# Kernel tuning notes

Hardware: AMD Instinct MI355X
Metric: run time of the kernel (lower is better)

Reference implementation:

```python
import jax, jax.numpy as jnp
import numpy as np

IMG_H = IMG_W = 640
NUM_CLASSES = 80
B = 8
NUM_ANCHORS = 76725
MAX_TOTAL = 200          # max_total_size == max_size_per_class
SCORE_TH = 0.5
IOU_TH = 0.5
K_CAND = 256             # per-class candidate pool for NMS (>= max survivors)
VARIANCES = jnp.asarray([0.1, 0.1, 0.2, 0.2], jnp.float32)


def _build_anchors(img_h, img_w):
    # RetinaNet AnchorBox: levels 3..7, 3 ratios x 3 scales, [cx, cy, w, h]
    ratios = [0.5, 1.0, 2.0]
    scales = [2.0 ** x for x in (0.0, 1.0 / 3.0, 2.0 / 3.0)]
    areas = [s * s for s in (32.0, 64.0, 128.0, 256.0, 512.0)]
    out = []
    for lvl, stride in enumerate([2 ** i for i in range(3, 8)]):
        dims = []
        for r in ratios:
            h = np.sqrt(areas[lvl] / r)
            w = areas[lvl] / h
            for s in scales:
                dims.append([w * s, h * s])
        dims = np.asarray(dims, np.float32)                      # [9,2]
        fh = int(np.ceil(img_h / stride)); fw = int(np.ceil(img_w / stride))
        rx = (np.arange(fw, dtype=np.float32) + 0.5) * stride
        ry = (np.arange(fh, dtype=np.float32) + 0.5) * stride
        cx, cy = np.meshgrid(rx, ry)
        centers = np.broadcast_to(np.stack([cx, cy], -1)[:, :, None, :], (fh, fw, 9, 2))
        d = np.broadcast_to(dims[None, None], (fh, fw, 9, 2))
        out.append(np.concatenate([centers, d], -1).reshape(-1, 4))
    return jnp.asarray(np.concatenate(out, 0))                   # [A,4]


def setup_inputs() -> dict:
    key = jax.random.key(0)
    k1, k2 = jax.random.split(key)
    box_pred = jax.random.normal(k1, (B, NUM_ANCHORS, 4), jnp.float32)
    cls_pred = jax.random.normal(k2, (B, NUM_ANCHORS, NUM_CLASSES), jnp.float32)
    anchor_boxes = _build_anchors(IMG_H, IMG_W)
    return {"box_pred": box_pred, "cls_pred": cls_pred, "anchor_boxes": anchor_boxes}


def _iou_one_vs_many(box, boxes):
    # box [4] vs boxes [K,4] in corner format
    lt = jnp.maximum(box[:2], boxes[:, :2])
    rb = jnp.minimum(box[2:], boxes[:, 2:])
    wh = jnp.maximum(rb - lt, 0.0)
    inter = wh[:, 0] * wh[:, 1]
    a1 = (box[2] - box[0]) * (box[3] - box[1])
    a2 = (boxes[:, 2] - boxes[:, 0]) * (boxes[:, 3] - boxes[:, 1])
    return inter / jnp.maximum(a1 + a2 - inter, 1e-8)


def _nms_keep(boxes, scores):
    # boxes [K,4] already sorted by descending score; greedy NMS
    eligible = scores > SCORE_TH
    idx = jnp.arange(K_CAND)

    def body(i, keep):
        iou = _iou_one_vs_many(boxes[i], boxes)
        suppress = (iou > IOU_TH) & (idx > i)
        return jnp.where(keep[i], keep & ~suppress, keep)

    keep = jax.lax.fori_loop(0, K_CAND, body, eligible)
    keep = keep & ((jnp.cumsum(keep) - 1) < MAX_TOTAL)           # max_size_per_class cap
    return keep


def _decode_and_nms(box_pred, cls_pred, anchor_boxes):
    scores_all = jax.nn.sigmoid(cls_pred)                        # [B,A,C]
    # decode: (dx,dy,dw,dh)*variances against [cx,cy,w,h] anchors
    d = box_pred * VARIANCES
    xy = d[..., :2] * anchor_boxes[None, :, 2:] + anchor_boxes[None, :, :2]
    wh = jnp.exp(d[..., 2:]) * anchor_boxes[None, :, 2:]
    boxes = jnp.concatenate([xy - 0.5 * wh, xy + 0.5 * wh], -1)  # [B,A,4] corners

    sc = jnp.swapaxes(scores_all, 1, 2)                          # [B,C,A]
    top_sc, top_idx = jax.lax.top_k(sc, K_CAND)                  # [B,C,K] sorted desc
    cand_boxes = jnp.take_along_axis(boxes[:, None], top_idx[..., None], axis=2)  # [B,C,K,4]

    keep = jax.lax.stop_gradient(jax.vmap(jax.vmap(_nms_keep))(cand_boxes, top_sc))  # [B,C,K]
    sel = jnp.where(keep, top_sc, -1.0)

    flat_sc = sel.reshape(B, -1)                                 # [B,C*K]
    flat_boxes = cand_boxes.reshape(B, -1, 4)
    flat_lbl = jnp.broadcast_to(jnp.arange(NUM_CLASSES)[None, :, None],
                                (B, NUM_CLASSES, K_CAND)).reshape(B, -1)

    fs, fi = jax.lax.top_k(flat_sc, MAX_TOTAL)                   # combine across classes
    out_boxes = jnp.take_along_axis(flat_boxes, fi[..., None], axis=1)
    out_lbl = jnp.take_along_axis(flat_lbl, fi, axis=1).astype(jnp.float32)
    valid = fs > 0.0                                             # pad invalid slots
    return (jnp.where(valid[..., None], out_boxes, 0.0),
            jnp.where(valid, fs, 0.0),
            jnp.where(valid, out_lbl, -1.0))


def reference(box_pred, cls_pred, anchor_boxes):
    return _decode_and_nms(box_pred, cls_pred, anchor_boxes)
```

## Files before the change

kernel.cpp:

```cpp
#include <hip/hip_runtime.h>
#include <math.h>
#include <stdint.h>

typedef unsigned long long u64;
typedef unsigned int u32;

#define NB 8
#define NA 76725
#define NC 80
#define KC 256
#define MAXT 200
#define CAP 2048
#define SELCAP 768
#define TAU 2.0f
#define CHUNK 512
#define NCHUNK 150
#define BCAP 48
#define CSTRIDE 16

#define OFF_BUFA      0ull
#define OFF_CLASSLIST 10485760ull
#define OFF_CANDBOX   11796480ull
#define OFF_COUNTS    14417920ull

__device__ __forceinline__ void kf_proc(float4 v, int i, int a0,
                                        u64 (*bucket)[BCAP], u32* bcnt) {
  int a = a0 + i / (NC / 4);
  int c0 = (i % (NC / 4)) * 4;
  float vv[4] = {v.x, v.y, v.z, v.w};
#pragma unroll
  for (int j = 0; j < 4; j++) {
    if (vv[j] > TAU) {
      int c = c0 + j;
      u32 pos = atomicAdd(&bcnt[c], 1u);
      if (pos < BCAP)
        bucket[c][pos] = ((u64)__float_as_uint(vv[j]) << 32) | (u32)a;
    }
  }
}

__global__ __launch_bounds__(256) void kfilter(const float* __restrict__ cls,
                                               u64* __restrict__ bufA,
                                               u32* __restrict__ counts) {
  __shared__ u64 bucket[NC][BCAP];
  __shared__ u32 bcnt[NC];
  __shared__ u32 gbase[NC];
  __shared__ u32 pref[NC + 1];

  const int b = blockIdx.x / NCHUNK;
  const int ch = blockIdx.x % NCHUNK;
  const int tid = threadIdx.x;
  const int a0 = ch * CHUNK;
  const int aN = (NA - a0) < CHUNK ? (NA - a0) : CHUNK;

  for (int i = tid; i < NC; i += 256) bcnt[i] = 0;
  __syncthreads();

  const float4* p = (const float4*)(cls + ((size_t)b * NA + a0) * NC);
  const int n4 = aN * (NC / 4);
  for (int i0 = tid; i0 < n4; i0 += 2048) {
    float4 v[8];
    bool g[8];
#pragma unroll
    for (int u = 0; u < 8; u++) {
      g[u] = (i0 + u * 256) < n4;
      if (g[u]) v[u] = p[i0 + u * 256];
    }
#pragma unroll
    for (int u = 0; u < 8; u++)
      if (g[u]) kf_proc(v[u], i0 + u * 256, a0, bucket, bcnt);
  }
  __syncthreads();
  if (tid < NC) {
    u32 n = bcnt[tid];
    if (n > BCAP) n = BCAP;
    bcnt[tid] = n;
    gbase[tid] = atomicAdd(&counts[(b * NC + tid) * CSTRIDE], n);
  }
  __syncthreads();
  if (tid == 0) {
    u32 s = 0;
    for (int c = 0; c < NC; c++) { pref[c] = s; s += bcnt[c]; }
    pref[NC] = s;
  }
  __syncthreads();
  const int total = (int)pref[NC];
  for (int e = tid; e < total; e += 256) {
    int lo = 0, hi = NC;
    while (lo + 1 < hi) { int mid = (lo + hi) >> 1; if ((int)pref[mid] <= e) lo = mid; else hi = mid; }
    int c = lo;
    int loc = e - (int)pref[c];
    u32 gb = gbase[c] + (u32)loc;
    if (gb < CAP)
      bufA[((size_t)(b * NC + c)) * CAP + gb] = bucket[c][loc];
  }
}

__global__ __launch_bounds__(256) void kselect(
    const float* __restrict__ cls, const float* __restrict__ boxp,
    const float* __restrict__ anc, u64* __restrict__ bufA,
    const u32* __restrict__ counts, u64* __restrict__ classList,
    float4* __restrict__ candBox) {
  __shared__ u64 sbuf[CAP];
  __shared__ u32 hist[1024];
  __shared__ u64 sel[SELCAP];
  __shared__ u64 skey[KC];
  __shared__ u64 scolT[4][KC];
  __shared__ float4 sBox[KC];
  __shared__ float sAr[KC];
  __shared__ int sNsel, sExtra, sSb;

  const int tid = threadIdx.x;
  const int bc = blockIdx.x;
  const int b = bc / NC, c = bc % NC;
  u64* buf = bufA + (size_t)bc * CAP;

  int cnt0 = (int)counts[bc * CSTRIDE];
  if (cnt0 > CAP) cnt0 = CAP;
  int cnt = cnt0;
  if (cnt0 < KC) {
    if (tid == 0) sExtra = 0;
    __syncthreads();
    for (int a = tid; a < NA; a += 256) {
      float x = cls[((size_t)b * NA + a) * NC + c];
      if (x > 0.0f && !(x > TAU)) {
        int pos = cnt0 + atomicAdd(&sExtra, 1);
        if (pos < CAP) buf[pos] = ((u64)__float_as_uint(x) << 32) | (u32)a;
      }
    }
    __syncthreads();
    cnt = cnt0 + sExtra;
  }
  if (cnt > CAP) cnt = CAP;

  for (int i = tid; i < 1024; i += 256) hist[i] = 0;
  if (tid == 0) sNsel = 0;
  skey[tid] = 0;
  for (int e = tid; e < cnt; e += 256) sbuf[e] = buf[e];
  __syncthreads();

  for (int e = tid; e < cnt; e += 256) {
    float f = __uint_as_float((u32)(sbuf[e] >> 32));
    int bin = (int)(f * 170.0f);
    bin = bin < 0 ? 0 : (bin > 1023 ? 1023 : bin);
    atomicAdd(&hist[bin], 1u);
  }
  __syncthreads();

  if (tid < 64) {
    int s = 0;
#pragma unroll
    for (int i = 0; i < 16; i++) s += (int)hist[tid * 16 + i];
    int suf = s;
#pragma unroll
    for (int d = 1; d < 64; d <<= 1) {
      int t = __shfl_down(suf, d, 64);
      if (tid + d < 64) suf += t;
    }
    u64 mask = __ballot(suf >= KC);
    int sb = mask ? (63 - __clzll((long long)mask)) : 0;
    if (tid == 0) sSb = sb;
  }
  __syncthreads();
  const int sb = sSb;

  for (int e = tid; e < cnt; e += 256) {
    u64 k = sbuf[e];
    float f = __uint_as_float((u32)(k >> 32));
    int bin = (int)(f * 170.0f);
    bin = bin < 0 ? 0 : (bin > 1023 ? 1023 : bin);
    if ((bin >> 4) >= sb) {
      float sc = 1.0f / (1.0f + expf(-f));
      u32 a = (u32)k;
      int pos = atomicAdd(&sNsel, 1);
      if (pos < SELCAP)
        sel[pos] = ((u64)__float_as_uint(sc) << 32) | (0xFFFFFFFFu - a);
    }
  }
  __syncthreads();
  int nsel = sNsel;
  if (nsel > SELCAP) nsel = SELCAP;

  for (int e = tid; e < nsel; e += 256) {
    u64 k = sel[e];
    int r = 0;
    for (int q = 0; q < nsel; q++) r += (sel[q] > k) ? 1 : 0;
    if (r < KC) skey[r] = k;
  }
  __syncthreads();

  {
    u64 k = skey[tid];
    u32 a = 0xFFFFFFFFu - (u32)k;
    if (k == 0ull || a >= NA) a = 0;
    float4 p = ((const float4*)boxp)[(size_t)b * NA + a];
    float4 an = ((const float4*)anc)[a];
    float dx = __fmul_rn(p.x, 0.1f), dy = __fmul_rn(p.y, 0.1f);
    float dw = __fmul_rn(p.z, 0.2f), dh = __fmul_rn(p.w, 0.2f);
    float cx = __fadd_rn(__fmul_rn(dx, an.z), an.x);
    float cy = __fadd_rn(__fmul_rn(dy, an.w), an.y);
    float w = __fmul_rn(expf(dw), an.z);
    float h = __fmul_rn(expf(dh), an.w);
    float4 bx;
    bx.x = __fsub_rn(cx, __fmul_rn(0.5f, w));
    bx.y = __fsub_rn(cy, __fmul_rn(0.5f, h));
    bx.z = __fadd_rn(cx, __fmul_rn(0.5f, w));
    bx.w = __fadd_rn(cy, __fmul_rn(0.5f, h));
    sBox[tid] = bx;
    sAr[tid] = __fmul_rn(__fsub_rn(bx.z, bx.x), __fsub_rn(bx.w, bx.y));
    candBox[(size_t)bc * KC + tid] = bx;
  }
  __syncthreads();

  {
    const int j = tid;
    float4 bj = sBox[j];
    float aj = sAr[j];
    u64 cw[4] = {0ull, 0ull, 0ull, 0ull};
    for (int i = 0; i < j; i++) {
      float4 bi = sBox[i];
      float ai = sAr[i];
      float lx = fmaxf(bi.x, bj.x), ly = fmaxf(bi.y, bj.y);
      float rx = fminf(bi.z, bj.z), ry = fminf(bi.w, bj.w);
      float wx = fmaxf(__fsub_rn(rx, lx), 0.0f);
      float wy = fmaxf(__fsub_rn(ry, ly), 0.0f);
      float inter = __fmul_rn(wx, wy);
      float uni = fmaxf(__fsub_rn(__fadd_rn(ai, aj), inter), 1e-8f);
      float iou = __fdiv_rn(inter, uni);
      if (iou > 0.5f) cw[i >> 6] |= (1ull << (i & 63));
    }
#pragma unroll
    for (int w = 0; w < 4; w++) scolT[w][j] = cw[w];
  }
  __syncthreads();

  if (tid < 64) {
    const int ln = tid;
    u64 C[4][4];
#pragma unroll
    for (int s = 0; s < 4; s++)
#pragma unroll
      for (int w = 0; w < 4; w++) C[s][w] = scolT[w][s * 64 + ln];
    int keep = 0;
#pragma unroll
    for (int s = 0; s < 4; s++)
      if (skey[s * 64 + ln] != 0ull) keep |= (1 << s);
#pragma unroll
    for (int w = 0; w < 4; w++) {
      u64 c0 = C[0][w], c1 = C[1][w], c2 = C[2][w], c3 = C[3][w];
      for (int t = 0; t < 64; t++) {
        int kt = __shfl(keep, t, 64);
        if ((kt >> w) & 1) {
          int sup = (int)((c0 >> t) & 1) | ((int)((c1 >> t) & 1) << 1) |
                    ((int)((c2 >> t) & 1) << 2) | ((int)((c3 >> t) & 1) << 3);
          keep &= ~sup;
        }
      }
    }
    u64 m[4];
#pragma unroll
    for (int s = 0; s < 4; s++) m[s] = __ballot((keep >> s) & 1);
    int tot = 0;
#pragma unroll
    for (int s = 0; s < 4; s++) tot += __popcll(m[s]);
    int keptTotal = tot < MAXT ? tot : MAXT;
    u64 lmask = (1ull << ln) - 1ull;
    int base = 0;
#pragma unroll
    for (int s = 0; s < 4; s++) {
      int j = s * 64 + ln;
      int cum = base + (int)__popcll(m[s] & lmask);
      if (((keep >> s) & 1) && cum < MAXT) {
        u64 hi = skey[j] >> 32;
        classList[(size_t)bc * KC + cum] =
            (hi << 32) | (u64)(0xFFFFFFFFu - (u32)(c * KC + j));
      }
      base += (int)__popcll(m[s]);
    }
    for (int t2 = ln; t2 < KC; t2 += 64)
      if (t2 >= keptTotal) classList[(size_t)bc * KC + t2] = 0;
  }
}

__device__ __forceinline__ u64 shfl64(u64 v, int src) {
  int lo = __shfl((int)(u32)v, src, 64);
  int hi = __shfl((int)(v >> 32), src, 64);
  return ((u64)(u32)hi << 32) | (u32)lo;
}
__device__ __forceinline__ u64 shflxor64(u64 v, int mask) {
  int lo = __shfl_xor((int)(u32)v, mask, 64);
  int hi = __shfl_xor((int)(v >> 32), mask, 64);
  return ((u64)(u32)hi << 32) | (u32)lo;
}
#define CSWAP(a, b) { if ((a) < (b)) { u64 _t = (a); (a) = (b); (b) = _t; } }

__device__ __forceinline__ void wave_merge(u64 acc[4], const u64 cur[4], int ln) {
  u64 t0 = shfl64(cur[3], 63 - ln);
  u64 t1 = shfl64(cur[2], 63 - ln);
  u64 t2 = shfl64(cur[1], 63 - ln);
  u64 t3 = shfl64(cur[0], 63 - ln);
  acc[0] = acc[0] > t0 ? acc[0] : t0;
  acc[1] = acc[1] > t1 ? acc[1] : t1;
  acc[2] = acc[2] > t2 ? acc[2] : t2;
  acc[3] = acc[3] > t3 ? acc[3] : t3;
  CSWAP(acc[0], acc[2]); CSWAP(acc[1], acc[3]);
  CSWAP(acc[0], acc[1]); CSWAP(acc[2], acc[3]);
#pragma unroll
  for (int s = 32; s >= 1; s >>= 1) {
#pragma unroll
    for (int k = 0; k < 4; k++) {
      u64 o = shflxor64(acc[k], s);
      u64 mx = acc[k] > o ? acc[k] : o;
      u64 mn = acc[k] < o ? acc[k] : o;
      acc[k] = ((ln & s) == 0) ? mx : mn;
    }
  }
}

__global__ __launch_bounds__(256) void kmerge(const u64* __restrict__ classList,
                                              const float4* __restrict__ candBox,
                                              float* __restrict__ out) {
  __shared__ u64 lds[4 * KC];
  const int tid = threadIdx.x, b = blockIdx.x;
  const int w = tid >> 6, ln = tid & 63;
  const u64* base = classList + ((size_t)b * NC + w * 20) * KC;
  u64 acc[4];
#pragma unroll
  for (int k = 0; k < 4; k++) acc[k] = base[k * 64 + ln];
  for (int m = 1; m < 20; m++) {
    u64 cur[4];
#pragma unroll
    for (int k = 0; k < 4; k++) cur[k] = base[(size_t)m * KC + k * 64 + ln];
    wave_merge(acc, cur, ln);
  }
#pragma unroll
  for (int k = 0; k < 4; k++) lds[w * KC + k * 64 + ln] = acc[k];
  __syncthreads();
  if (w == 0) {
    for (int m = 1; m < 4; m++) {
      u64 cur[4];
#pragma unroll
      for (int k = 0; k < 4; k++) cur[k] = lds[m * KC + k * 64 + ln];
      wave_merge(acc, cur, ln);
    }
#pragma unroll
    for (int k = 0; k < 4; k++) lds[k * 64 + ln] = acc[k];
  }
  __syncthreads();
  if (tid < MAXT) {
    u64 k = lds[tid];
    float4 bx = make_float4(0.f, 0.f, 0.f, 0.f);
    float sc = 0.0f, lb = -1.0f;
    if (k != 0ull) {
      sc = __uint_as_float((u32)(k >> 32));
      u32 flat = 0xFFFFFFFFu - (u32)k;
      int cc = (int)(flat >> 8), kk = (int)(flat & 255u);
      bx = candBox[((size_t)b * NC + cc) * KC + kk];
      lb = (float)cc;
    }
    float* ob = out + ((size_t)b * MAXT + tid) * 4;
    ob[0] = bx.x; ob[1] = bx.y; ob[2] = bx.z; ob[3] = bx.w;
    out[NB * MAXT * 4 + b * MAXT + tid] = sc;
    out[NB * MAXT * 4 + NB * MAXT + b * MAXT + tid] = lb;
  }
}

extern "C" void kernel_launch(void* const* d_in, const int* in_sizes, int n_in,
                              void* d_out, int out_size, void* d_ws,
                              size_t ws_size, hipStream_t stream) {
  const float* boxp = (const float*)d_in[0];
  const float* cls = (const float*)d_in[1];
  const float* anc = (const float*)d_in[2];
  char* ws = (char*)d_ws;
  u64* bufA = (u64*)(ws + OFF_BUFA);
  u64* classList = (u64*)(ws + OFF_CLASSLIST);
  float4* candBox = (float4*)(ws + OFF_CANDBOX);
  u32* counts = (u32*)(ws + OFF_COUNTS);

  hipMemsetAsync(counts, 0, NB * NC * CSTRIDE * sizeof(u32), stream);
  kfilter<<<NB * NCHUNK, 256, 0, stream>>>(cls, bufA, counts);
  kselect<<<NB * NC, 256, 0, stream>>>(cls, boxp, anc, bufA, counts, classList,
                                       candBox);
  kmerge<<<NB, 256, 0, stream>>>(classList, candBox, (float*)d_out);
}
```

Measured before the change: 392.6 us.

## Alias shared-memory buffers and skip NMS rows that suppress nothing

Overlays the kselect kernel's shared arrays onto one 24 KB buffer, reusing regions whose lifetimes do not overlap. This cuts LDS use per block and may allow more resident blocks. It also builds, with wave shuffles and atomics, a mask of candidate rows that suppress at least one later box. The serial NMS sweep then visits only those rows instead of all 64 per word. The cost is extra shuffle and atomic work in the IoU phase, plus correctness depending on the aliased regions really being dead when overwritten.

Result: faster. 372.5 us (-5.1%).

```diff
diff --git a/kernel.cpp b/kernel.cpp
--- a/kernel.cpp
+++ b/kernel.cpp
@@ -101,13 +101,15 @@
     const float* __restrict__ anc, u64* __restrict__ bufA,
     const u32* __restrict__ counts, u64* __restrict__ classList,
     float4* __restrict__ candBox) {
-  __shared__ u64 sbuf[CAP];
-  __shared__ u32 hist[1024];
-  __shared__ u64 sel[SELCAP];
-  __shared__ u64 skey[KC];
-  __shared__ u64 scolT[4][KC];
-  __shared__ float4 sBox[KC];
-  __shared__ float sAr[KC];
+  __shared__ __align__(16) char smem[24576];
+  u64* sbuf = (u64*)smem;
+  u64 (*scolT)[KC] = (u64(*)[KC])smem;
+  float4* sBox = (float4*)(smem + 8192);
+  float* sAr = (float*)(smem + 12288);
+  u32* hist = (u32*)(smem + 16384);
+  u64* sel = (u64*)(smem + 16384);
+  u64* skey = (u64*)(smem + 22528);
+  __shared__ u32 sRowAnyLo[4], sRowAnyHi[4];
   __shared__ int sNsel, sExtra, sSb;
 
   const int tid = threadIdx.x;
@@ -190,6 +192,7 @@
   __syncthreads();
 
   {
+    if (tid < 4) { sRowAnyLo[tid] = 0; sRowAnyHi[tid] = 0; }
     u64 k = skey[tid];
     u32 a = 0xFFFFFFFFu - (u32)k;
     if (k == 0ull || a >= NA) a = 0;
@@ -231,6 +234,20 @@
     }
 #pragma unroll
     for (int w = 0; w < 4; w++) scolT[w][j] = cw[w];
+#pragma unroll
+    for (int w = 0; w < 4; w++) {
+      u64 r = cw[w];
+#pragma unroll
+      for (int m = 1; m < 64; m <<= 1) {
+        int lo = __shfl_xor((int)(u32)r, m, 64);
+        int hi = __shfl_xor((int)(r >> 32), m, 64);
+        r |= ((u64)(u32)hi << 32) | (u32)lo;
+      }
+      if ((tid & 63) == 0) {
+        atomicOr(&sRowAnyLo[w], (u32)r);
+        atomicOr(&sRowAnyHi[w], (u32)(r >> 32));
+      }
+    }
   }
   __syncthreads();
 
@@ -248,7 +265,10 @@
 #pragma unroll
     for (int w = 0; w < 4; w++) {
       u64 c0 = C[0][w], c1 = C[1][w], c2 = C[2][w], c3 = C[3][w];
-      for (int t = 0; t < 64; t++) {
+      u64 rw = ((u64)sRowAnyHi[w] << 32) | (u64)sRowAnyLo[w];
+      while (rw) {
+        int t = __builtin_ctzll(rw);
+        rw &= rw - 1;
         int kt = __shfl(keep, t, 64);
         if ((kt >> w) & 1) {
           int sup = (int)((c0 >> t) & 1) | ((int)((c1 >> t) & 1) << 1) |
```
